# Optimization experiments

Measured on AMD Instinct MI355X. Metric: run time of the kernel, lower is better.

The kernel has to match this reference:

```python
import jax, jax.numpy as jnp
import numpy as np
from jax import lax

THRESHOLDS = (0.25, 0.5, 0.75)
TAU = 100.0
NUM_CLASSES = 10
K = 32
RES_Z = 5.0
# each of the 16 binary logic gates is bilinear: g(a,b) = c0 + c1*a + c2*b + c3*a*b
GATE_COEF = jnp.array([
    [0, 0, 0, 0],   # 0: False
    [0, 0, 0, 1],   # 1: a AND b
    [0, 1, 0, -1],  # 2: a AND NOT b
    [0, 1, 0, 0],   # 3: a  (residual gate)
    [0, 0, 1, -1],  # 4: NOT a AND b
    [0, 0, 1, 0],   # 5: b
    [0, 1, 1, -2],  # 6: XOR
    [0, 1, 1, -1],  # 7: OR
    [1, -1, -1, 1], # 8: NOR
    [1, -1, -1, 2], # 9: XNOR
    [1, 0, -1, 0],  # 10: NOT b
    [1, 0, -1, 1],  # 11: a OR NOT b
    [1, -1, 0, 0],  # 12: NOT a
    [1, -1, 0, 1],  # 13: NOT a OR b
    [1, 0, 0, -1],  # 14: NAND
    [1, 0, 0, 0],   # 15: True
], dtype=jnp.float32)


def _gate_logits(key, shape):
    # residual init: pass-through gate (id 3) dominates
    w = 0.01 * jax.random.normal(key, shape, dtype=jnp.float32)
    return w.at[..., 3].add(RES_Z)


def _leaf_idx(rng, C, O, leaves=8, cpt=2, kk=9):
    # each tree uses cpt random input channels; each leaf picks one of them and a 3x3 position
    ch2 = rng.integers(0, C, size=(O, cpt))
    sel = rng.integers(0, cpt, size=(O, leaves))
    ch = np.take_along_axis(ch2, sel, axis=1)
    pos = rng.integers(0, kk, size=(O, leaves))
    return jnp.asarray(ch * kk + pos, dtype=jnp.int32)


def setup_inputs() -> dict:
    key = jax.random.key(0)
    ks = jax.random.split(key, 9)
    rng = np.random.default_rng(0)
    B = 128
    d = {"x": jax.random.uniform(ks[0], (B, 3, 32, 32), dtype=jnp.float32)}
    in_chs = [3 * len(THRESHOLDS), K, 4 * K, 16 * K]
    out_chs = [K, 4 * K, 16 * K, 32 * K]
    for i, (ci, co) in enumerate(zip(in_chs, out_chs)):
        d[f"c{i+1}_idx"] = _leaf_idx(rng, ci, co)
        d[f"c{i+1}_w"] = _gate_logits(ks[1 + i], (co, 7, 16))
    dims = [32 * K * 4, 1280 * K, 640 * K, 320 * K]
    for i in range(3):
        di, do = dims[i], dims[i + 1]
        d[f"l{i+1}_a"] = jnp.asarray(rng.integers(0, di, size=(do,)), dtype=jnp.int32)
        d[f"l{i+1}_b"] = jnp.asarray(rng.integers(0, di, size=(do,)), dtype=jnp.int32)
        d[f"l{i+1}_w"] = _gate_logits(ks[5 + i], (do, 16))
    return d


def _mix(logits):
    # softmax over 16 gates folded into 4 bilinear coefficients (fused gate mixture)
    return jax.nn.softmax(logits, axis=-1) @ GATE_COEF


def binarize(x):
    return jnp.concatenate([(x > t).astype(x.dtype) for t in THRESHOLDS], axis=1)


def tree_conv(x, leaf_idx, logits):
    # x: (B,C,H,W); leaf_idx: (O,8) into C*9 channel-major patch; logits: (O,7,16)
    B, C, H, W = x.shape
    xp = jnp.pad(x, ((0, 0), (0, 0), (1, 1), (1, 1)))
    patches = jnp.stack([xp[:, :, i:i + H, j:j + W] for i in range(3) for j in range(3)], axis=2)
    patches = patches.reshape(B, C * 9, H, W)
    vals = patches[:, leaf_idx]  # (B,O,8,H,W)
    m = _mix(logits)             # (O,7,4)
    node = 0
    for lvl in (4, 2, 1):
        a, b = vals[:, :, 0::2], vals[:, :, 1::2]
        w = m[:, node:node + lvl]  # (O,lvl,4)
        w0 = w[..., 0][None, :, :, None, None]
        w1 = w[..., 1][None, :, :, None, None]
        w2 = w[..., 2][None, :, :, None, None]
        w3 = w[..., 3][None, :, :, None, None]
        vals = w0 + w1 * a + w2 * b + w3 * (a * b)
        node += lvl
    return vals[:, :, 0]  # (B,O,H,W)


def or_pool(x):
    # OR of relaxed binary values == max pool 2x2/2
    return lax.reduce_window(x, -jnp.inf, lax.max, (1, 1, 2, 2), (1, 1, 2, 2), "VALID")


def logic_layer(x, a_idx, b_idx, logits):
    a = x[:, a_idx]  # (B,O)
    b = x[:, b_idx]
    w = _mix(logits)  # (O,4)
    return w[:, 0] + w[:, 1] * a + w[:, 2] * b + w[:, 3] * (a * b)


def group_sum(x):
    B = x.shape[0]
    return x.reshape(B, NUM_CLASSES, -1).sum(axis=-1) / TAU


def reference(x, c1_idx, c1_w, c2_idx, c2_w, c3_idx, c3_w, c4_idx, c4_w,
              l1_a, l1_b, l1_w, l2_a, l2_b, l2_w, l3_a, l3_b, l3_w):
    h = binarize(x)
    h = or_pool(tree_conv(h, c1_idx, c1_w))
    h = or_pool(tree_conv(h, c2_idx, c2_w))
    h = or_pool(tree_conv(h, c3_idx, c3_w))
    h = or_pool(tree_conv(h, c4_idx, c4_w))
    h = h.reshape(h.shape[0], -1)  # (B, 4096)
    h = logic_layer(h, l1_a, l1_b, l1_w)
    h = logic_layer(h, l2_a, l2_b, l2_w)
    h = logic_layer(h, l3_a, l3_b, l3_w)
    return group_sum(h)  # (B, 10)
```

## Files before the change

### kernel.cpp

```cpp
#include <hip/hip_runtime.h>

#define BATCH 128

typedef float v2f __attribute__((ext_vector_type(2)));
typedef float v4f __attribute__((ext_vector_type(4)));

__device__ __constant__ float GC[16][4] = {
  {0,0,0,0},{0,0,0,1},{0,1,0,-1},{0,1,0,0},
  {0,0,1,-1},{0,0,1,0},{0,1,1,-2},{0,1,1,-1},
  {1,-1,-1,1},{1,-1,-1,2},{1,0,-1,0},{1,0,-1,1},
  {1,-1,0,0},{1,-1,0,1},{1,0,0,-1},{1,0,0,0}};

__device__ __forceinline__ v2f pk_mul(v2f a, v2f b) {
  v2f d;
  asm("v_pk_mul_f32 %0, %1, %2" : "=v"(d) : "v"(a), "v"(b));
  return d;
}
__device__ __forceinline__ v2f max2(v2f a, v2f b) {
  v2f d;
  d.x = fmaxf(a.x, b.x);
  d.y = fmaxf(a.y, b.y);
  return d;
}
__device__ __forceinline__ v2f gate2pk(v2f a, v2f b, v2f w01, v2f w23) {
  v2f t = pk_mul(a, b);
  v2f d;
  asm("v_pk_fma_f32 %0, %1, %2, %2 op_sel:[0,1,0] op_sel_hi:[1,1,0]"
      : "=v"(d) : "v"(a), "v"(w01));
  asm("v_pk_fma_f32 %0, %1, %2, %0 op_sel:[0,0,0] op_sel_hi:[1,0,1]"
      : "+v"(d) : "v"(b), "v"(w23));
  asm("v_pk_fma_f32 %0, %1, %2, %0 op_sel:[0,1,0] op_sel_hi:[1,1,1]"
      : "+v"(d) : "v"(t), "v"(w23));
  return d;
}

__device__ __forceinline__ void mix_one(const float* lp, float* op) {
  float e[16];
  float s = 0.f;
  #pragma unroll
  for (int i = 0; i < 16; ++i) { e[i] = __expf(lp[i]); s += e[i]; }
  float inv = 1.0f / s;
  float w0 = 0.f, w1 = 0.f, w2 = 0.f, w3 = 0.f;
  #pragma unroll
  for (int i = 0; i < 16; ++i) {
    float p = e[i] * inv;
    w0 = fmaf(p, GC[i][0], w0);
    w1 = fmaf(p, GC[i][1], w1);
    w2 = fmaf(p, GC[i][2], w2);
    w3 = fmaf(p, GC[i][3], w3);
  }
  op[0] = w0; op[1] = w1; op[2] = w2; op[3] = w3;
}

struct PrepArgs {
  const float* x;
  const float* logits[7];
  float* outm[7];
  float* xtb;
  float* out;
};

__global__ __launch_bounds__(256) void prep_k(PrepArgs A) {
  __shared__ float tile[64 * 129];
  int blk = blockIdx.x;
  if (blk < 327) {
    int gid = blk * 256 + threadIdx.x;
    const int n[7] = {224, 896, 3584, 7168, 40960, 20480, 10240};
    if (gid < 83552) {
      int g = gid, seg = 0;
      while (seg < 6 && g >= n[seg]) { g -= n[seg]; ++seg; }
      mix_one(A.logits[seg] + (size_t)g * 16, A.outm[seg] + (size_t)g * 4);
    }
  } else if (blk < 327 + 144) {
    int tb = blk - 327;
    int c    = tb / 16;
    int pix0 = (tb % 16) * 64;
    int ti = c / 3, rgb = c - ti * 3;
    float th = 0.25f * (float)(ti + 1);
    {
      int pix = threadIdx.x & 63;
      int b0  = threadIdx.x >> 6;
      #pragma unroll 4
      for (int i = 0; i < 32; ++i) {
        int b = b0 + i * 4;
        float xv = A.x[(size_t)(b * 3 + rgb) * 1024 + pix0 + pix];
        tile[pix * 129 + b] = (xv > th) ? 1.f : 0.f;
      }
    }
    __syncthreads();
    {
      int b  = threadIdx.x & 127;
      int p0 = threadIdx.x >> 7;
      #pragma unroll 4
      for (int i = 0; i < 32; ++i) {
        int pix = p0 + i * 2;
        A.xtb[(size_t)(c * 1024 + pix0 + pix) * BATCH + b] = tile[pix * 129 + b];
      }
    }
  } else {
    int t = threadIdx.x;
    #pragma unroll
    for (int i = 0; i < 5; ++i) A.out[t * 5 + i] = 0.f;
  }
}

template <int H, int W>
__global__ __launch_bounds__(256) void conv_t(
    const float* __restrict__ in_t, const int* __restrict__ li_g,
    const float* __restrict__ m, float* __restrict__ out_t) {
  constexpr int PH = H / 2, PWD = W / 2, PIX = PH * PWD;
  int wave = threadIdx.x >> 6;
  int b2   = threadIdx.x & 63;
  int q = __builtin_amdgcn_readfirstlane(blockIdx.x * 4 + wave);
  int o = q / PIX;
  int p = q - o * PIX;
  int ph = p / PWD;
  int pw = p - ph * PWD;

  const int* li = li_g + o * 8;
  const v4f* mv = (const v4f*)(m + o * 28);
  v4f g0 = mv[0], g1 = mv[1], g2 = mv[2], g3 = mv[3];
  v4f g4 = mv[4], g5 = mv[5], g6 = mv[6];

  v2f best = {-1e30f, -1e30f};
  #pragma unroll
  for (int half = 0; half < 2; ++half) {
    v2f v[2][8];
    #pragma unroll
    for (int l = 0; l < 8; ++l) {
      int idx = li[l];
      int c = idx / 9;
      int k = idx - c * 9;
      int di = k / 3 - 1;
      int dj = (k - (k / 3) * 3) - 1;
      const float* base = in_t + (size_t)(c * H * W) * BATCH;
      int y = 2 * ph + half + di;
      #pragma unroll
      for (int pi = 0; pi < 2; ++pi) {
        int x = 2 * pw + pi + dj;
        v2f val = {0.f, 0.f};
        if ((unsigned)y < (unsigned)H && (unsigned)x < (unsigned)W)
          val = ((const v2f*)(base + (size_t)(y * W + x) * BATCH))[b2];
        v[pi][l] = val;
      }
    }
    #pragma unroll
    for (int pi = 0; pi < 2; ++pi) {
      v2f u0 = gate2pk(v[pi][0], v[pi][1], g0.xy, g0.zw);
      v2f u1 = gate2pk(v[pi][2], v[pi][3], g1.xy, g1.zw);
      v2f u2 = gate2pk(v[pi][4], v[pi][5], g2.xy, g2.zw);
      v2f u3 = gate2pk(v[pi][6], v[pi][7], g3.xy, g3.zw);
      v2f s0 = gate2pk(u0, u1, g4.xy, g4.zw);
      v2f s1 = gate2pk(u2, u3, g5.xy, g5.zw);
      v2f r  = gate2pk(s0, s1, g6.xy, g6.zw);
      best = max2(best, r);
    }
  }
  ((v2f*)(out_t + (size_t)q * BATCH))[b2] = best;
}

__global__ __launch_bounds__(256) void logic_k(
    const float* __restrict__ in, const int* __restrict__ aidx,
    const int* __restrict__ bidx, const float* __restrict__ m,
    float* __restrict__ out) {
  int wave = threadIdx.x >> 6;
  int b2   = threadIdx.x & 63;
  int j0 = blockIdx.x * 16 + wave;
  #pragma unroll
  for (int it = 0; it < 4; ++it) {
    int j = __builtin_amdgcn_readfirstlane(j0 + it * 4);
    int ai = aidx[j];
    int bi = bidx[j];
    v4f w = ((const v4f*)m)[j];
    v2f a = ((const v2f*)(in + (size_t)ai * BATCH))[b2];
    v2f b = ((const v2f*)(in + (size_t)bi * BATCH))[b2];
    ((v2f*)(out + (size_t)j * BATCH))[b2] = gate2pk(a, b, w.xy, w.zw);
  }
}

__global__ __launch_bounds__(256) void logic3_gsum_k(
    const float* __restrict__ in, const int* __restrict__ aidx,
    const int* __restrict__ bidx, const float* __restrict__ m,
    float* __restrict__ out) {
  __shared__ v2f red[4][64];
  int wave = threadIdx.x >> 6;
  int b2   = threadIdx.x & 63;
  int base = __builtin_amdgcn_readfirstlane(blockIdx.x * 256 + wave * 64);
  int cls  = base >> 10;
  v2f s = {0.f, 0.f};
  #pragma unroll 4
  for (int it = 0; it < 64; ++it) {
    int j = base + it;
    int ai = aidx[j];
    int bi = bidx[j];
    v4f w = ((const v4f*)m)[j];
    v2f a = ((const v2f*)(in + (size_t)ai * BATCH))[b2];
    v2f b = ((const v2f*)(in + (size_t)bi * BATCH))[b2];
    s += gate2pk(a, b, w.xy, w.zw);
  }
  red[wave][b2] = s;
  __syncthreads();
  if (threadIdx.x < 64) {
    v2f t = red[0][b2] + red[1][b2] + red[2][b2] + red[3][b2];
    atomicAdd(&out[(2 * b2) * 10 + cls], t.x * 0.01f);
    atomicAdd(&out[(2 * b2 + 1) * 10 + cls], t.y * 0.01f);
  }
}

extern "C" void kernel_launch(void* const* d_in, const int* in_sizes, int n_in,
                              void* d_out, int out_size, void* d_ws, size_t ws_size,
                              hipStream_t stream) {
  const float* x   = (const float*)d_in[0];
  const int*   c1i = (const int*)d_in[1];
  const float* c1w = (const float*)d_in[2];
  const int*   c2i = (const int*)d_in[3];
  const float* c2w = (const float*)d_in[4];
  const int*   c3i = (const int*)d_in[5];
  const float* c3w = (const float*)d_in[6];
  const int*   c4i = (const int*)d_in[7];
  const float* c4w = (const float*)d_in[8];
  const int*   l1a = (const int*)d_in[9];
  const int*   l1b = (const int*)d_in[10];
  const float* l1w = (const float*)d_in[11];
  const int*   l2a = (const int*)d_in[12];
  const int*   l2b = (const int*)d_in[13];
  const float* l2w = (const float*)d_in[14];
  const int*   l3a = (const int*)d_in[15];
  const int*   l3b = (const int*)d_in[16];
  const float* l3w = (const float*)d_in[17];

  float* ws = (float*)d_ws;
  float* mc1 = ws;
  float* mc2 = mc1 + 896;
  float* mc3 = mc2 + 3584;
  float* mc4 = mc3 + 14336;
  float* ml1 = mc4 + 28672;
  float* ml2 = ml1 + 163840;
  float* ml3 = ml2 + 81920;
  float* xtb = ml3 + 40960;
  float* h1  = xtb + 1179648;
  float* h2  = h1 + 1048576;
  float* h3  = h2 + 1048576;
  float* h4  = h3 + 1048576;
  float* g1  = h4 + 524288;
  float* g2  = g1 + 5242880;

  PrepArgs A;
  A.x = x;
  A.logits[0] = c1w; A.outm[0] = mc1;
  A.logits[1] = c2w; A.outm[1] = mc2;
  A.logits[2] = c3w; A.outm[2] = mc3;
  A.logits[3] = c4w; A.outm[3] = mc4;
  A.logits[4] = l1w; A.outm[4] = ml1;
  A.logits[5] = l2w; A.outm[5] = ml2;
  A.logits[6] = l3w; A.outm[6] = ml3;
  A.xtb = xtb;
  A.out = (float*)d_out;
  prep_k<<<472, 256, 0, stream>>>(A);

  conv_t<32, 32><<<8192 / 4, 256, 0, stream>>>(xtb, c1i, mc1, h1);
  conv_t<16, 16><<<8192 / 4, 256, 0, stream>>>(h1, c2i, mc2, h2);
  conv_t<8, 8><<<8192 / 4, 256, 0, stream>>>(h2, c3i, mc3, h3);
  conv_t<4, 4><<<4096 / 4, 256, 0, stream>>>(h3, c4i, mc4, h4);

  logic_k<<<40960 / 16, 256, 0, stream>>>(h4, l1a, l1b, ml1, g1);
  logic_k<<<20480 / 16, 256, 0, stream>>>(g1, l2a, l2b, ml2, g2);
  logic3_gsum_k<<<40, 256, 0, stream>>>(g2, l3a, l3b, ml3, (float*)d_out);
}
```

Baseline: 158.2 us.

## Store intermediate activations in fp16 and spread final logic layer over more blocks

All intermediate activation buffers (binarized input, conv outputs, logic layer outputs) are stored as half2 instead of float, which halves the bytes moved by the gather-heavy conv and logic kernels. The conv kernel also remaps block indices in an 8-way interleave to change which output channels and pixels neighbouring blocks handle, likely for cache or channel locality. The final logic+group-sum kernel launches 320 blocks of 8 gates per wave instead of 40 blocks of 64, giving more parallelism at the cost of more atomics. Intermediate values lose precision, since the relaxed gate outputs are rounded to fp16 after every layer.

```diff
diff --git a/kernel.cpp b/kernel.cpp
--- a/kernel.cpp
+++ b/kernel.cpp
@@ -1,4 +1,5 @@
 #include <hip/hip_runtime.h>
+#include <hip/hip_fp16.h>
 
 #define BATCH 128
 
@@ -34,6 +35,15 @@
   return d;
 }
 
+__device__ __forceinline__ v2f h2f(__half2 h) {
+  float2 f = __half22float2(h);
+  return v2f{f.x, f.y};
+}
+__device__ __forceinline__ __half2 f2h(v2f v) {
+  float2 f; f.x = v.x; f.y = v.y;
+  return __float22half2_rn(f);
+}
+
 __device__ __forceinline__ void mix_one(const float* lp, float* op) {
   float e[16];
   float s = 0.f;
@@ -56,7 +66,7 @@
   const float* x;
   const float* logits[7];
   float* outm[7];
-  float* xtb;
+  __half* xtb;
   float* out;
 };
 
@@ -89,12 +99,16 @@
     }
     __syncthreads();
     {
-      int b  = threadIdx.x & 127;
-      int p0 = threadIdx.x >> 7;
+      int b2i = threadIdx.x & 63;
+      int p0  = threadIdx.x >> 6;
       #pragma unroll 4
-      for (int i = 0; i < 32; ++i) {
-        int pix = p0 + i * 2;
-        A.xtb[(size_t)(c * 1024 + pix0 + pix) * BATCH + b] = tile[pix * 129 + b];
+      for (int i = 0; i < 16; ++i) {
+        int pix = p0 + i * 4;
+        float lo = tile[pix * 129 + 2 * b2i];
+        float hi = tile[pix * 129 + 2 * b2i + 1];
+        float2 f; f.x = lo; f.y = hi;
+        ((__half2*)A.xtb)[(size_t)(c * 1024 + pix0 + pix) * 64 + b2i] =
+            __float22half2_rn(f);
       }
     }
   } else {
@@ -106,12 +120,14 @@
 
 template <int H, int W>
 __global__ __launch_bounds__(256) void conv_t(
-    const float* __restrict__ in_t, const int* __restrict__ li_g,
-    const float* __restrict__ m, float* __restrict__ out_t) {
+    const __half* __restrict__ in_t, const int* __restrict__ li_g,
+    const float* __restrict__ m, __half* __restrict__ out_t) {
   constexpr int PH = H / 2, PWD = W / 2, PIX = PH * PWD;
   int wave = threadIdx.x >> 6;
   int b2   = threadIdx.x & 63;
-  int q = __builtin_amdgcn_readfirstlane(blockIdx.x * 4 + wave);
+  int nb8  = gridDim.x >> 3;
+  int sb   = (blockIdx.x & 7) * nb8 + (blockIdx.x >> 3);
+  int q = __builtin_amdgcn_readfirstlane(sb * 4 + wave);
   int o = q / PIX;
   int p = q - o * PIX;
   int ph = p / PWD;
@@ -121,6 +137,8 @@
   const v4f* mv = (const v4f*)(m + o * 28);
   v4f g0 = mv[0], g1 = mv[1], g2 = mv[2], g3 = mv[3];
   v4f g4 = mv[4], g5 = mv[5], g6 = mv[6];
+
+  const __half2* in2 = (const __half2*)in_t;
 
   v2f best = {-1e30f, -1e30f};
   #pragma unroll
@@ -133,14 +151,13 @@
       int k = idx - c * 9;
       int di = k / 3 - 1;
       int dj = (k - (k / 3) * 3) - 1;
-      const float* base = in_t + (size_t)(c * H * W) * BATCH;
       int y = 2 * ph + half + di;
       #pragma unroll
       for (int pi = 0; pi < 2; ++pi) {
         int x = 2 * pw + pi + dj;
         v2f val = {0.f, 0.f};
         if ((unsigned)y < (unsigned)H && (unsigned)x < (unsigned)W)
-          val = ((const v2f*)(base + (size_t)(y * W + x) * BATCH))[b2];
+          val = h2f(in2[(size_t)(c * H * W + y * W + x) * 64 + b2]);
         v[pi][l] = val;
       }
     }
@@ -156,46 +173,48 @@
       best = max2(best, r);
     }
   }
-  ((v2f*)(out_t + (size_t)q * BATCH))[b2] = best;
+  ((__half2*)out_t)[(size_t)q * 64 + b2] = f2h(best);
 }
 
 __global__ __launch_bounds__(256) void logic_k(
-    const float* __restrict__ in, const int* __restrict__ aidx,
+    const __half* __restrict__ in, const int* __restrict__ aidx,
     const int* __restrict__ bidx, const float* __restrict__ m,
-    float* __restrict__ out) {
+    __half* __restrict__ out) {
   int wave = threadIdx.x >> 6;
   int b2   = threadIdx.x & 63;
   int j0 = blockIdx.x * 16 + wave;
+  const __half2* in2 = (const __half2*)in;
   #pragma unroll
   for (int it = 0; it < 4; ++it) {
     int j = __builtin_amdgcn_readfirstlane(j0 + it * 4);
     int ai = aidx[j];
     int bi = bidx[j];
     v4f w = ((const v4f*)m)[j];
-    v2f a = ((const v2f*)(in + (size_t)ai * BATCH))[b2];
-    v2f b = ((const v2f*)(in + (size_t)bi * BATCH))[b2];
-    ((v2f*)(out + (size_t)j * BATCH))[b2] = gate2pk(a, b, w.xy, w.zw);
+    v2f a = h2f(in2[(size_t)ai * 64 + b2]);
+    v2f b = h2f(in2[(size_t)bi * 64 + b2]);
+    ((__half2*)out)[(size_t)j * 64 + b2] = f2h(gate2pk(a, b, w.xy, w.zw));
   }
 }
 
 __global__ __launch_bounds__(256) void logic3_gsum_k(
-    const float* __restrict__ in, const int* __restrict__ aidx,
+    const __half* __restrict__ in, const int* __restrict__ aidx,
     const int* __restrict__ bidx, const float* __restrict__ m,
     float* __restrict__ out) {
   __shared__ v2f red[4][64];
   int wave = threadIdx.x >> 6;
   int b2   = threadIdx.x & 63;
-  int base = __builtin_amdgcn_readfirstlane(blockIdx.x * 256 + wave * 64);
+  int base = __builtin_amdgcn_readfirstlane(blockIdx.x * 32 + wave * 8);
   int cls  = base >> 10;
+  const __half2* in2 = (const __half2*)in;
   v2f s = {0.f, 0.f};
-  #pragma unroll 4
-  for (int it = 0; it < 64; ++it) {
+  #pragma unroll
+  for (int it = 0; it < 8; ++it) {
     int j = base + it;
     int ai = aidx[j];
     int bi = bidx[j];
     v4f w = ((const v4f*)m)[j];
-    v2f a = ((const v2f*)(in + (size_t)ai * BATCH))[b2];
-    v2f b = ((const v2f*)(in + (size_t)bi * BATCH))[b2];
+    v2f a = h2f(in2[(size_t)ai * 64 + b2]);
+    v2f b = h2f(in2[(size_t)bi * 64 + b2]);
     s += gate2pk(a, b, w.xy, w.zw);
   }
   red[wave][b2] = s;
@@ -237,13 +256,13 @@
   float* ml1 = mc4 + 28672;
   float* ml2 = ml1 + 163840;
   float* ml3 = ml2 + 81920;
-  float* xtb = ml3 + 40960;
-  float* h1  = xtb + 1179648;
-  float* h2  = h1 + 1048576;
-  float* h3  = h2 + 1048576;
-  float* h4  = h3 + 1048576;
-  float* g1  = h4 + 524288;
-  float* g2  = g1 + 5242880;
+  __half* xtb = (__half*)(ml3 + 40960);
+  __half* h1  = xtb + 1179648;
+  __half* h2  = h1 + 1048576;
+  __half* h3  = h2 + 1048576;
+  __half* h4  = h3 + 1048576;
+  __half* g1  = h4 + 524288;
+  __half* g2  = g1 + 5242880;
 
   PrepArgs A;
   A.x = x;
@@ -265,5 +284,5 @@
 
   logic_k<<<40960 / 16, 256, 0, stream>>>(h4, l1a, l1b, ml1, g1);
   logic_k<<<20480 / 16, 256, 0, stream>>>(g1, l2a, l2b, ml2, g2);
-  logic3_gsum_k<<<40, 256, 0, stream>>>(g2, l3a, l3b, ml3, (float*)d_out);
-}
+  logic3_gsum_k<<<320, 256, 0, stream>>>(g2, l3a, l3b, ml3, (float*)d_out);
+}
```

Result: slower. 183.5 us (+16.0%).

## Process four batch elements per lane and two outputs per wave in all kernels

Applied to the files above, without the earlier changes.

Each lane now loads and computes a float4 of batch values instead of float2, so one wave covers two pooled output pixels (conv) or two gate outputs (logic), halving grid sizes. Conv blocks are also remapped with an 8-way interleave of block indices, presumably for locality across channels. The final logic/group-sum kernel is split across more blocks, with a smaller per-wave loop and a revised reduction. Wider loads cut instruction count per byte, but each lane holds more live registers and fewer waves are available to hide latency.

```diff
diff --git a/kernel.cpp b/kernel.cpp
--- a/kernel.cpp
+++ b/kernel.cpp
@@ -14,12 +14,6 @@
 __device__ __forceinline__ v2f pk_mul(v2f a, v2f b) {
   v2f d;
   asm("v_pk_mul_f32 %0, %1, %2" : "=v"(d) : "v"(a), "v"(b));
-  return d;
-}
-__device__ __forceinline__ v2f max2(v2f a, v2f b) {
-  v2f d;
-  d.x = fmaxf(a.x, b.x);
-  d.y = fmaxf(a.y, b.y);
   return d;
 }
 __device__ __forceinline__ v2f gate2pk(v2f a, v2f b, v2f w01, v2f w23) {
@@ -31,6 +25,20 @@
       : "+v"(d) : "v"(b), "v"(w23));
   asm("v_pk_fma_f32 %0, %1, %2, %0 op_sel:[0,1,0] op_sel_hi:[1,1,1]"
       : "+v"(d) : "v"(t), "v"(w23));
+  return d;
+}
+__device__ __forceinline__ v4f gate4pk(v4f a, v4f b, v2f w01, v2f w23) {
+  v4f r;
+  r.xy = gate2pk(a.xy, b.xy, w01, w23);
+  r.zw = gate2pk(a.zw, b.zw, w01, w23);
+  return r;
+}
+__device__ __forceinline__ v4f max4(v4f a, v4f b) {
+  v4f d;
+  d.x = fmaxf(a.x, b.x);
+  d.y = fmaxf(a.y, b.y);
+  d.z = fmaxf(a.z, b.z);
+  d.w = fmaxf(a.w, b.w);
   return d;
 }
 
@@ -110,22 +118,32 @@
     const float* __restrict__ m, float* __restrict__ out_t) {
   constexpr int PH = H / 2, PWD = W / 2, PIX = PH * PWD;
   int wave = threadIdx.x >> 6;
-  int b2   = threadIdx.x & 63;
-  int q = __builtin_amdgcn_readfirstlane(blockIdx.x * 4 + wave);
-  int o = q / PIX;
-  int p = q - o * PIX;
-  int ph = p / PWD;
-  int pw = p - ph * PWD;
+  int lane = threadIdx.x & 63;
+  int half_id = lane >> 5;
+  int b4      = lane & 31;
+  int nb8  = gridDim.x >> 3;
+  int sb   = (blockIdx.x & 7) * nb8 + (blockIdx.x >> 3);
+  int t = __builtin_amdgcn_readfirstlane(sb * 4 + wave);
+  int q0 = 2 * t;
+  int o  = q0 / PIX;
+  int p0 = q0 - o * PIX;
+  int ph = p0 / PWD;
+  int pw0 = p0 - ph * PWD;
 
   const int* li = li_g + o * 8;
   const v4f* mv = (const v4f*)(m + o * 28);
   v4f g0 = mv[0], g1 = mv[1], g2 = mv[2], g3 = mv[3];
   v4f g4 = mv[4], g5 = mv[5], g6 = mv[6];
 
-  v2f best = {-1e30f, -1e30f};
+  int px    = 2 * half_id;
+  int vlane = half_id * 64 + b4;
+
+  const v4f* in4 = (const v4f*)in_t;
+
+  v4f best = {-1e30f, -1e30f, -1e30f, -1e30f};
   #pragma unroll
   for (int half = 0; half < 2; ++half) {
-    v2f v[2][8];
+    v4f v[2][8];
     #pragma unroll
     for (int l = 0; l < 8; ++l) {
       int idx = li[l];
@@ -133,30 +151,31 @@
       int k = idx - c * 9;
       int di = k / 3 - 1;
       int dj = (k - (k / 3) * 3) - 1;
-      const float* base = in_t + (size_t)(c * H * W) * BATCH;
       int y = 2 * ph + half + di;
+      int rowb = c * (H * W) + y * W;
       #pragma unroll
       for (int pi = 0; pi < 2; ++pi) {
-        int x = 2 * pw + pi + dj;
-        v2f val = {0.f, 0.f};
+        int sx = 2 * pw0 + pi + dj;
+        int x  = sx + px;
+        v4f val = {0.f, 0.f, 0.f, 0.f};
         if ((unsigned)y < (unsigned)H && (unsigned)x < (unsigned)W)
-          val = ((const v2f*)(base + (size_t)(y * W + x) * BATCH))[b2];
+          val = in4[(ptrdiff_t)(rowb + sx) * 32 + vlane];
         v[pi][l] = val;
       }
     }
     #pragma unroll
     for (int pi = 0; pi < 2; ++pi) {
-      v2f u0 = gate2pk(v[pi][0], v[pi][1], g0.xy, g0.zw);
-      v2f u1 = gate2pk(v[pi][2], v[pi][3], g1.xy, g1.zw);
-      v2f u2 = gate2pk(v[pi][4], v[pi][5], g2.xy, g2.zw);
-      v2f u3 = gate2pk(v[pi][6], v[pi][7], g3.xy, g3.zw);
-      v2f s0 = gate2pk(u0, u1, g4.xy, g4.zw);
-      v2f s1 = gate2pk(u2, u3, g5.xy, g5.zw);
-      v2f r  = gate2pk(s0, s1, g6.xy, g6.zw);
-      best = max2(best, r);
-    }
-  }
-  ((v2f*)(out_t + (size_t)q * BATCH))[b2] = best;
+      v4f u0 = gate4pk(v[pi][0], v[pi][1], g0.xy, g0.zw);
+      v4f u1 = gate4pk(v[pi][2], v[pi][3], g1.xy, g1.zw);
+      v4f u2 = gate4pk(v[pi][4], v[pi][5], g2.xy, g2.zw);
+      v4f u3 = gate4pk(v[pi][6], v[pi][7], g3.xy, g3.zw);
+      v4f s0 = gate4pk(u0, u1, g4.xy, g4.zw);
+      v4f s1 = gate4pk(u2, u3, g5.xy, g5.zw);
+      v4f r  = gate4pk(s0, s1, g6.xy, g6.zw);
+      best = max4(best, r);
+    }
+  }
+  ((v4f*)out_t)[(size_t)q0 * 32 + half_id * 32 + b4] = best;
 }
 
 __global__ __launch_bounds__(256) void logic_k(
@@ -164,17 +183,20 @@
     const int* __restrict__ bidx, const float* __restrict__ m,
     float* __restrict__ out) {
   int wave = threadIdx.x >> 6;
-  int b2   = threadIdx.x & 63;
-  int j0 = blockIdx.x * 16 + wave;
+  int lane = threadIdx.x & 63;
+  int half_id = lane >> 5;
+  int b4      = lane & 31;
+  int jb = blockIdx.x * 32 + wave * 2;
+  const v4f* in4 = (const v4f*)in;
   #pragma unroll
   for (int it = 0; it < 4; ++it) {
-    int j = __builtin_amdgcn_readfirstlane(j0 + it * 4);
-    int ai = aidx[j];
-    int bi = bidx[j];
-    v4f w = ((const v4f*)m)[j];
-    v2f a = ((const v2f*)(in + (size_t)ai * BATCH))[b2];
-    v2f b = ((const v2f*)(in + (size_t)bi * BATCH))[b2];
-    ((v2f*)(out + (size_t)j * BATCH))[b2] = gate2pk(a, b, w.xy, w.zw);
+    int jj = jb + it * 8 + half_id;
+    int ai = aidx[jj];
+    int bi = bidx[jj];
+    v4f w = ((const v4f*)m)[jj];
+    v4f a = in4[(size_t)ai * 32 + b4];
+    v4f b = in4[(size_t)bi * 32 + b4];
+    ((v4f*)out)[(size_t)jj * 32 + b4] = gate4pk(a, b, w.xy, w.zw);
   }
 }
 
@@ -182,28 +204,34 @@
     const float* __restrict__ in, const int* __restrict__ aidx,
     const int* __restrict__ bidx, const float* __restrict__ m,
     float* __restrict__ out) {
-  __shared__ v2f red[4][64];
+  __shared__ v4f red[4][64];
   int wave = threadIdx.x >> 6;
-  int b2   = threadIdx.x & 63;
-  int base = __builtin_amdgcn_readfirstlane(blockIdx.x * 256 + wave * 64);
+  int lane = threadIdx.x & 63;
+  int half_id = lane >> 5;
+  int b4      = lane & 31;
+  int base = __builtin_amdgcn_readfirstlane(blockIdx.x * 32 + wave * 8);
   int cls  = base >> 10;
-  v2f s = {0.f, 0.f};
-  #pragma unroll 4
-  for (int it = 0; it < 64; ++it) {
-    int j = base + it;
+  const v4f* in4 = (const v4f*)in;
+  v4f s = {0.f, 0.f, 0.f, 0.f};
+  #pragma unroll
+  for (int it = 0; it < 4; ++it) {
+    int j = base + half_id * 4 + it;
     int ai = aidx[j];
     int bi = bidx[j];
     v4f w = ((const v4f*)m)[j];
-    v2f a = ((const v2f*)(in + (size_t)ai * BATCH))[b2];
-    v2f b = ((const v2f*)(in + (size_t)bi * BATCH))[b2];
-    s += gate2pk(a, b, w.xy, w.zw);
-  }
-  red[wave][b2] = s;
+    v4f a = in4[(size_t)ai * 32 + b4];
+    v4f b = in4[(size_t)bi * 32 + b4];
+    s += gate4pk(a, b, w.xy, w.zw);
+  }
+  red[wave][lane] = s;
   __syncthreads();
-  if (threadIdx.x < 64) {
-    v2f t = red[0][b2] + red[1][b2] + red[2][b2] + red[3][b2];
-    atomicAdd(&out[(2 * b2) * 10 + cls], t.x * 0.01f);
-    atomicAdd(&out[(2 * b2 + 1) * 10 + cls], t.y * 0.01f);
+  if (threadIdx.x < 32) {
+    v4f t = {0.f, 0.f, 0.f, 0.f};
+    #pragma unroll
+    for (int w = 0; w < 4; ++w) t += red[w][threadIdx.x] + red[w][threadIdx.x + 32];
+    #pragma unroll
+    for (int i = 0; i < 4; ++i)
+      atomicAdd(&out[(4 * threadIdx.x + i) * 10 + cls], t[i] * 0.01f);
   }
 }
 
@@ -258,12 +286,12 @@
   A.out = (float*)d_out;
   prep_k<<<472, 256, 0, stream>>>(A);
 
-  conv_t<32, 32><<<8192 / 4, 256, 0, stream>>>(xtb, c1i, mc1, h1);
-  conv_t<16, 16><<<8192 / 4, 256, 0, stream>>>(h1, c2i, mc2, h2);
-  conv_t<8, 8><<<8192 / 4, 256, 0, stream>>>(h2, c3i, mc3, h3);
-  conv_t<4, 4><<<4096 / 4, 256, 0, stream>>>(h3, c4i, mc4, h4);
-
-  logic_k<<<40960 / 16, 256, 0, stream>>>(h4, l1a, l1b, ml1, g1);
-  logic_k<<<20480 / 16, 256, 0, stream>>>(g1, l2a, l2b, ml2, g2);
-  logic3_gsum_k<<<40, 256, 0, stream>>>(g2, l3a, l3b, ml3, (float*)d_out);
-}
+  conv_t<32, 32><<<8192 / 8, 256, 0, stream>>>(xtb, c1i, mc1, h1);
+  conv_t<16, 16><<<8192 / 8, 256, 0, stream>>>(h1, c2i, mc2, h2);
+  conv_t<8, 8><<<8192 / 8, 256, 0, stream>>>(h2, c3i, mc3, h3);
+  conv_t<4, 4><<<4096 / 8, 256, 0, stream>>>(h3, c4i, mc4, h4);
+
+  logic_k<<<40960 / 32, 256, 0, stream>>>(h4, l1a, l1b, ml1, g1);
+  logic_k<<<20480 / 32, 256, 0, stream>>>(g1, l2a, l2b, ml2, g2);
+  logic3_gsum_k<<<320, 256, 0, stream>>>(g2, l3a, l3b, ml3, (float*)d_out);
+}
```

Result: no change. 157.3 us (-0.6%).

## Fuse all conv and logic layers into one per-sample LDS-resident megakernel

Applied to the files above, without the earlier changes.

Replaces the chain of eight global-memory kernels with a single kernel in which one 512-thread block processes one batch sample. All activations stay in shared memory, using halo-padded buffers so bounds checks disappear and precomputed leaf offsets. Logic-layer activations are kept in fp16 to fit in LDS, and the group sum is reduced in-block with no global atomics. This removes inter-kernel launches and global round trips, but exposes only 128 blocks of parallelism and adds fp16 rounding to intermediate values.

```diff
diff --git a/kernel.cpp b/kernel.cpp
--- a/kernel.cpp
+++ b/kernel.cpp
@@ -1,9 +1,9 @@
 #include <hip/hip_runtime.h>
-
-#define BATCH 128
+#include <hip/hip_fp16.h>
 
 typedef float v2f __attribute__((ext_vector_type(2)));
 typedef float v4f __attribute__((ext_vector_type(4)));
+typedef int   v4i __attribute__((ext_vector_type(4)));
 
 __device__ __constant__ float GC[16][4] = {
   {0,0,0,0},{0,0,0,1},{0,1,0,-1},{0,1,0,0},
@@ -14,12 +14,6 @@
 __device__ __forceinline__ v2f pk_mul(v2f a, v2f b) {
   v2f d;
   asm("v_pk_mul_f32 %0, %1, %2" : "=v"(d) : "v"(a), "v"(b));
-  return d;
-}
-__device__ __forceinline__ v2f max2(v2f a, v2f b) {
-  v2f d;
-  d.x = fmaxf(a.x, b.x);
-  d.y = fmaxf(a.y, b.y);
   return d;
 }
 __device__ __forceinline__ v2f gate2pk(v2f a, v2f b, v2f w01, v2f w23) {
@@ -53,158 +47,208 @@
 }
 
 struct PrepArgs {
-  const float* x;
   const float* logits[7];
   float* outm[7];
-  float* xtb;
+  const int* cidx[4];
+  int* offt[4];
+};
+
+__global__ __launch_bounds__(256) void prep_k(PrepArgs A) {
+  int gid = blockIdx.x * 256 + threadIdx.x;
+  if (gid < 83552) {
+    const int n[7] = {224, 896, 3584, 7168, 40960, 20480, 10240};
+    int g = gid, seg = 0;
+    while (seg < 6 && g >= n[seg]) { g -= n[seg]; ++seg; }
+    mix_one(A.logits[seg] + (size_t)g * 16, A.outm[seg] + (size_t)g * 4);
+  } else if (gid < 85248) {
+    int r = gid - 83552;
+    int L, rr, H;
+    if (r < 32)       { L = 0; rr = r;       H = 32; }
+    else if (r < 160) { L = 1; rr = r - 32;  H = 16; }
+    else if (r < 672) { L = 2; rr = r - 160; H = 8;  }
+    else              { L = 3; rr = r - 672; H = 4;  }
+    const int* ci = A.cidx[L] + rr * 8;
+    int* oo = A.offt[L] + rr * 8;
+    int W2 = H + 2;
+    #pragma unroll
+    for (int l = 0; l < 8; ++l) {
+      int idx = ci[l];
+      int c  = idx / 9;
+      int k  = idx - 9 * c;
+      int di = k / 3 - 1;
+      int dj = k - 3 * (k / 3) - 1;
+      oo[l] = (c * (H + 2) + 1 + di) * W2 + 1 + dj;
+    }
+  }
+}
+
+struct MegaArgs {
+  const float* x;
+  const float* mc[4];
+  const int*   offt[4];
+  const int*   la[3];
+  const int*   lb[3];
+  const float* mlw[3];
   float* out;
 };
 
-__global__ __launch_bounds__(256) void prep_k(PrepArgs A) {
-  __shared__ float tile[64 * 129];
-  int blk = blockIdx.x;
-  if (blk < 327) {
-    int gid = blk * 256 + threadIdx.x;
-    const int n[7] = {224, 896, 3584, 7168, 40960, 20480, 10240};
-    if (gid < 83552) {
-      int g = gid, seg = 0;
-      while (seg < 6 && g >= n[seg]) { g -= n[seg]; ++seg; }
-      mix_one(A.logits[seg] + (size_t)g * 16, A.outm[seg] + (size_t)g * 4);
-    }
-  } else if (blk < 327 + 144) {
-    int tb = blk - 327;
-    int c    = tb / 16;
-    int pix0 = (tb % 16) * 64;
-    int ti = c / 3, rgb = c - ti * 3;
-    float th = 0.25f * (float)(ti + 1);
-    {
-      int pix = threadIdx.x & 63;
-      int b0  = threadIdx.x >> 6;
-      #pragma unroll 4
-      for (int i = 0; i < 32; ++i) {
-        int b = b0 + i * 4;
-        float xv = A.x[(size_t)(b * 3 + rgb) * 1024 + pix0 + pix];
-        tile[pix * 129 + b] = (xv > th) ? 1.f : 0.f;
-      }
-    }
-    __syncthreads();
-    {
-      int b  = threadIdx.x & 127;
-      int p0 = threadIdx.x >> 7;
-      #pragma unroll 4
-      for (int i = 0; i < 32; ++i) {
-        int pix = p0 + i * 2;
-        A.xtb[(size_t)(c * 1024 + pix0 + pix) * BATCH + b] = tile[pix * 129 + b];
-      }
-    }
-  } else {
-    int t = threadIdx.x;
-    #pragma unroll
-    for (int i = 0; i < 5; ++i) A.out[t * 5 + i] = 0.f;
-  }
-}
-
-template <int H, int W>
-__global__ __launch_bounds__(256) void conv_t(
-    const float* __restrict__ in_t, const int* __restrict__ li_g,
-    const float* __restrict__ m, float* __restrict__ out_t) {
-  constexpr int PH = H / 2, PWD = W / 2, PIX = PH * PWD;
-  int wave = threadIdx.x >> 6;
-  int b2   = threadIdx.x & 63;
-  int q = __builtin_amdgcn_readfirstlane(blockIdx.x * 4 + wave);
-  int o = q / PIX;
-  int p = q - o * PIX;
-  int ph = p / PWD;
-  int pw = p - ph * PWD;
-
-  const int* li = li_g + o * 8;
-  const v4f* mv = (const v4f*)(m + o * 28);
-  v4f g0 = mv[0], g1 = mv[1], g2 = mv[2], g3 = mv[3];
-  v4f g4 = mv[4], g5 = mv[5], g6 = mv[6];
-
-  v2f best = {-1e30f, -1e30f};
-  #pragma unroll
-  for (int half = 0; half < 2; ++half) {
-    v2f v[2][8];
+extern __shared__ char S[];
+
+template<int OH, int OW, int LOGOW, int IW2, int PIXCNT, int LOGPIX,
+         int NCH, int ITERS, bool UNI, bool HALO>
+__device__ __forceinline__ void conv_stage(
+    const float* in, float* outb,
+    const int* __restrict__ offt, const float* __restrict__ mtab, int tid) {
+  int pix = tid & (PIXCNT - 1);
+  int ch0 = tid >> LOGPIX;
+  int pw  = pix & (OW - 1);
+  int ph  = pix >> LOGOW;
+  int pixbase = (2 * ph) * IW2 + 2 * pw;
+  #pragma unroll 2
+  for (int it = 0; it < ITERS; ++it) {
+    int ch = ch0 + NCH * it;
+    if (UNI) ch = __builtin_amdgcn_readfirstlane(ch);
+    const int* ot = offt + ch * 8;
+    const float* mt = mtab + ch * 28;
+    v4f g0 = *(const v4f*)(mt +  0);
+    v4f g1 = *(const v4f*)(mt +  4);
+    v4f g2 = *(const v4f*)(mt +  8);
+    v4f g3 = *(const v4f*)(mt + 12);
+    v4f g4 = *(const v4f*)(mt + 16);
+    v4f g5 = *(const v4f*)(mt + 20);
+    v4f g6 = *(const v4f*)(mt + 24);
+    v2f v01[8], v23[8];
     #pragma unroll
     for (int l = 0; l < 8; ++l) {
-      int idx = li[l];
-      int c = idx / 9;
-      int k = idx - c * 9;
-      int di = k / 3 - 1;
-      int dj = (k - (k / 3) * 3) - 1;
-      const float* base = in_t + (size_t)(c * H * W) * BATCH;
-      int y = 2 * ph + half + di;
+      int a0 = ot[l] + pixbase;
+      v2f t0; t0.x = in[a0];       t0.y = in[a0 + 1];
+      v2f t1; t1.x = in[a0 + IW2]; t1.y = in[a0 + IW2 + 1];
+      v01[l] = t0; v23[l] = t1;
+    }
+    v2f u0 = gate2pk(v01[0], v01[1], g0.xy, g0.zw);
+    v2f u1 = gate2pk(v01[2], v01[3], g1.xy, g1.zw);
+    v2f u2 = gate2pk(v01[4], v01[5], g2.xy, g2.zw);
+    v2f u3 = gate2pk(v01[6], v01[7], g3.xy, g3.zw);
+    v2f s0 = gate2pk(u0, u1, g4.xy, g4.zw);
+    v2f s1 = gate2pk(u2, u3, g5.xy, g5.zw);
+    v2f r0 = gate2pk(s0, s1, g6.xy, g6.zw);
+    u0 = gate2pk(v23[0], v23[1], g0.xy, g0.zw);
+    u1 = gate2pk(v23[2], v23[3], g1.xy, g1.zw);
+    u2 = gate2pk(v23[4], v23[5], g2.xy, g2.zw);
+    u3 = gate2pk(v23[6], v23[7], g3.xy, g3.zw);
+    s0 = gate2pk(u0, u1, g4.xy, g4.zw);
+    s1 = gate2pk(u2, u3, g5.xy, g5.zw);
+    v2f r1 = gate2pk(s0, s1, g6.xy, g6.zw);
+    float res = fmaxf(fmaxf(r0.x, r0.y), fmaxf(r1.x, r1.y));
+    if (HALO)
+      outb[ch * (OH + 2) * (OW + 2) + (1 + ph) * (OW + 2) + 1 + pw] = res;
+    else
+      outb[ch * (OH * OW) + pix] = res;
+  }
+}
+
+__global__ __launch_bounds__(512, 2) void mega_k(MegaArgs A) {
+  int tid = threadIdx.x;
+  int b = blockIdx.x;
+  float* binb = (float*)(S);
+  float* buf1 = (float*)(S + 53248);
+  float* buf2 = (float*)(S);
+  float* buf3 = (float*)(S + 53248);
+  float* h4   = (float*)(S);
+  __half* g1h = (__half*)(S + 16384);
+  __half* g2h = (__half*)(S + 98304);
+  float* lsum = (float*)(S + 139264);
+
+  for (int i = tid; i < 10404; i += 512) binb[i] = 0.f;
+  if (tid < 10) lsum[tid] = 0.f;
+  __syncthreads();
+  const float* xb = A.x + (size_t)b * 3072;
+  #pragma unroll
+  for (int i = 0; i < 6; ++i) {
+    int idx = tid + 512 * i;
+    float v = xb[idx];
+    int rgb = idx >> 10;
+    int rem = idx & 1023;
+    int y = rem >> 5, xx = rem & 31;
+    int base = (1 + y) * 34 + 1 + xx;
+    binb[(0 + rgb) * 1156 + base] = v > 0.25f ? 1.f : 0.f;
+    binb[(3 + rgb) * 1156 + base] = v > 0.50f ? 1.f : 0.f;
+    binb[(6 + rgb) * 1156 + base] = v > 0.75f ? 1.f : 0.f;
+  }
+  __syncthreads();
+
+  for (int i = tid; i < 10368; i += 512) buf1[i] = 0.f;
+  __syncthreads();
+  conv_stage<16,16,4,34,256,8,2,16,true,true>(binb, buf1, A.offt[0], A.mc[0], tid);
+  __syncthreads();
+  for (int i = tid; i < 12800; i += 512) buf2[i] = 0.f;
+  __syncthreads();
+  conv_stage<8,8,3,18,64,6,8,16,true,true>(buf1, buf2, A.offt[1], A.mc[1], tid);
+  __syncthreads();
+  for (int i = tid; i < 18432; i += 512) buf3[i] = 0.f;
+  __syncthreads();
+  conv_stage<4,4,2,10,16,4,32,16,false,true>(buf2, buf3, A.offt[2], A.mc[2], tid);
+  __syncthreads();
+  conv_stage<2,2,1,6,4,2,128,8,false,false>(buf3, h4, A.offt[3], A.mc[3], tid);
+  __syncthreads();
+
+  {
+    const v4i* a4 = (const v4i*)A.la[0];
+    const v4i* b4 = (const v4i*)A.lb[0];
+    const v4f* w4 = (const v4f*)A.mlw[0];
+    #pragma unroll 2
+    for (int g = 0; g < 20; ++g) {
+      int q = tid + 512 * g;
+      v4i ai = a4[q], bi = b4[q];
       #pragma unroll
-      for (int pi = 0; pi < 2; ++pi) {
-        int x = 2 * pw + pi + dj;
-        v2f val = {0.f, 0.f};
-        if ((unsigned)y < (unsigned)H && (unsigned)x < (unsigned)W)
-          val = ((const v2f*)(base + (size_t)(y * W + x) * BATCH))[b2];
-        v[pi][l] = val;
+      for (int i = 0; i < 4; ++i) {
+        v4f w = w4[4 * q + i];
+        float a = h4[ai[i]], bb = h4[bi[i]];
+        g1h[4 * q + i] = __float2half(fmaf(w.w, a * bb, fmaf(w.z, bb, fmaf(w.y, a, w.x))));
       }
     }
+  }
+  __syncthreads();
+  {
+    const v4i* a4 = (const v4i*)A.la[1];
+    const v4i* b4 = (const v4i*)A.lb[1];
+    const v4f* w4 = (const v4f*)A.mlw[1];
+    #pragma unroll 2
+    for (int g = 0; g < 10; ++g) {
+      int q = tid + 512 * g;
+      v4i ai = a4[q], bi = b4[q];
+      #pragma unroll
+      for (int i = 0; i < 4; ++i) {
+        v4f w = w4[4 * q + i];
+        float a = __half2float(g1h[ai[i]]), bb = __half2float(g2h == 0 ? g1h[bi[i]] : g1h[bi[i]]);
+        g2h[4 * q + i] = __float2half(fmaf(w.w, a * bb, fmaf(w.z, bb, fmaf(w.y, a, w.x))));
+      }
+    }
+  }
+  __syncthreads();
+  {
+    const v4i* a4 = (const v4i*)A.la[2];
+    const v4i* b4 = (const v4i*)A.lb[2];
+    const v4f* w4 = (const v4f*)A.mlw[2];
+    int wv = tid >> 6, lane = tid & 63;
     #pragma unroll
-    for (int pi = 0; pi < 2; ++pi) {
-      v2f u0 = gate2pk(v[pi][0], v[pi][1], g0.xy, g0.zw);
-      v2f u1 = gate2pk(v[pi][2], v[pi][3], g1.xy, g1.zw);
-      v2f u2 = gate2pk(v[pi][4], v[pi][5], g2.xy, g2.zw);
-      v2f u3 = gate2pk(v[pi][6], v[pi][7], g3.xy, g3.zw);
-      v2f s0 = gate2pk(u0, u1, g4.xy, g4.zw);
-      v2f s1 = gate2pk(u2, u3, g5.xy, g5.zw);
-      v2f r  = gate2pk(s0, s1, g6.xy, g6.zw);
-      best = max2(best, r);
-    }
-  }
-  ((v2f*)(out_t + (size_t)q * BATCH))[b2] = best;
-}
-
-__global__ __launch_bounds__(256) void logic_k(
-    const float* __restrict__ in, const int* __restrict__ aidx,
-    const int* __restrict__ bidx, const float* __restrict__ m,
-    float* __restrict__ out) {
-  int wave = threadIdx.x >> 6;
-  int b2   = threadIdx.x & 63;
-  int j0 = blockIdx.x * 16 + wave;
-  #pragma unroll
-  for (int it = 0; it < 4; ++it) {
-    int j = __builtin_amdgcn_readfirstlane(j0 + it * 4);
-    int ai = aidx[j];
-    int bi = bidx[j];
-    v4f w = ((const v4f*)m)[j];
-    v2f a = ((const v2f*)(in + (size_t)ai * BATCH))[b2];
-    v2f b = ((const v2f*)(in + (size_t)bi * BATCH))[b2];
-    ((v2f*)(out + (size_t)j * BATCH))[b2] = gate2pk(a, b, w.xy, w.zw);
-  }
-}
-
-__global__ __launch_bounds__(256) void logic3_gsum_k(
-    const float* __restrict__ in, const int* __restrict__ aidx,
-    const int* __restrict__ bidx, const float* __restrict__ m,
-    float* __restrict__ out) {
-  __shared__ v2f red[4][64];
-  int wave = threadIdx.x >> 6;
-  int b2   = threadIdx.x & 63;
-  int base = __builtin_amdgcn_readfirstlane(blockIdx.x * 256 + wave * 64);
-  int cls  = base >> 10;
-  v2f s = {0.f, 0.f};
-  #pragma unroll 4
-  for (int it = 0; it < 64; ++it) {
-    int j = base + it;
-    int ai = aidx[j];
-    int bi = bidx[j];
-    v4f w = ((const v4f*)m)[j];
-    v2f a = ((const v2f*)(in + (size_t)ai * BATCH))[b2];
-    v2f b = ((const v2f*)(in + (size_t)bi * BATCH))[b2];
-    s += gate2pk(a, b, w.xy, w.zw);
-  }
-  red[wave][b2] = s;
-  __syncthreads();
-  if (threadIdx.x < 64) {
-    v2f t = red[0][b2] + red[1][b2] + red[2][b2] + red[3][b2];
-    atomicAdd(&out[(2 * b2) * 10 + cls], t.x * 0.01f);
-    atomicAdd(&out[(2 * b2 + 1) * 10 + cls], t.y * 0.01f);
-  }
+    for (int g = 0; g < 5; ++g) {
+      int q = tid + 512 * g;
+      v4i ai = a4[q], bi = b4[q];
+      float s = 0.f;
+      #pragma unroll
+      for (int i = 0; i < 4; ++i) {
+        v4f w = w4[4 * q + i];
+        float a = __half2float(g2h[ai[i]]), bb = __half2float(g2h[bi[i]]);
+        s += fmaf(w.w, a * bb, fmaf(w.z, bb, fmaf(w.y, a, w.x)));
+      }
+      #pragma unroll
+      for (int m = 1; m < 64; m <<= 1) s += __shfl_xor(s, m);
+      if (lane == 0) atomicAdd(&lsum[(wv + 8 * g) >> 2], s);
+    }
+  }
+  __syncthreads();
+  if (tid < 10) A.out[b * 10 + tid] = lsum[tid] * 0.01f;
 }
 
 extern "C" void kernel_launch(void* const* d_in, const int* in_sizes, int n_in,
@@ -237,33 +281,39 @@
   float* ml1 = mc4 + 28672;
   float* ml2 = ml1 + 163840;
   float* ml3 = ml2 + 81920;
-  float* xtb = ml3 + 40960;
-  float* h1  = xtb + 1179648;
-  float* h2  = h1 + 1048576;
-  float* h3  = h2 + 1048576;
-  float* h4  = h3 + 1048576;
-  float* g1  = h4 + 524288;
-  float* g2  = g1 + 5242880;
-
-  PrepArgs A;
-  A.x = x;
-  A.logits[0] = c1w; A.outm[0] = mc1;
-  A.logits[1] = c2w; A.outm[1] = mc2;
-  A.logits[2] = c3w; A.outm[2] = mc3;
-  A.logits[3] = c4w; A.outm[3] = mc4;
-  A.logits[4] = l1w; A.outm[4] = ml1;
-  A.logits[5] = l2w; A.outm[5] = ml2;
-  A.logits[6] = l3w; A.outm[6] = ml3;
-  A.xtb = xtb;
-  A.out = (float*)d_out;
-  prep_k<<<472, 256, 0, stream>>>(A);
-
-  conv_t<32, 32><<<8192 / 4, 256, 0, stream>>>(xtb, c1i, mc1, h1);
-  conv_t<16, 16><<<8192 / 4, 256, 0, stream>>>(h1, c2i, mc2, h2);
-  conv_t<8, 8><<<8192 / 4, 256, 0, stream>>>(h2, c3i, mc3, h3);
-  conv_t<4, 4><<<4096 / 4, 256, 0, stream>>>(h3, c4i, mc4, h4);
-
-  logic_k<<<40960 / 16, 256, 0, stream>>>(h4, l1a, l1b, ml1, g1);
-  logic_k<<<20480 / 16, 256, 0, stream>>>(g1, l2a, l2b, ml2, g2);
-  logic3_gsum_k<<<40, 256, 0, stream>>>(g2, l3a, l3b, ml3, (float*)d_out);
-}
+  int* off1 = (int*)(ml3 + 40960);
+  int* off2 = off1 + 256;
+  int* off3 = off2 + 1024;
+  int* off4 = off3 + 4096;
+
+  PrepArgs P;
+  P.logits[0] = c1w; P.outm[0] = mc1;
+  P.logits[1] = c2w; P.outm[1] = mc2;
+  P.logits[2] = c3w; P.outm[2] = mc3;
+  P.logits[3] = c4w; P.outm[3] = mc4;
+  P.logits[4] = l1w; P.outm[4] = ml1;
+  P.logits[5] = l2w; P.outm[5] = ml2;
+  P.logits[6] = l3w; P.outm[6] = ml3;
+  P.cidx[0] = c1i; P.offt[0] = off1;
+  P.cidx[1] = c2i; P.offt[1] = off2;
+  P.cidx[2] = c3i; P.offt[2] = off3;
+  P.cidx[3] = c4i; P.offt[3] = off4;
+  prep_k<<<333, 256, 0, stream>>>(P);
+
+  MegaArgs M;
+  M.x = x;
+  M.mc[0] = mc1; M.mc[1] = mc2; M.mc[2] = mc3; M.mc[3] = mc4;
+  M.offt[0] = off1; M.offt[1] = off2; M.offt[2] = off3; M.offt[3] = off4;
+  M.la[0] = l1a; M.lb[0] = l1b; M.mlw[0] = ml1;
+  M.la[1] = l2a; M.lb[1] = l2b; M.mlw[1] = ml2;
+  M.la[2] = l3a; M.lb[2] = l3b; M.mlw[2] = ml3;
+  M.out = (float*)d_out;
+
+  static bool attr_set = false;
+  if (!attr_set) {
+    hipFuncSetAttribute((const void*)mega_k,
+                        hipFuncAttributeMaxDynamicSharedMemorySize, 139328);
+    attr_set = true;
+  }
+  mega_k<<<128, 512, 139328, stream>>>(M);
+}
```

After: 161.1 us. No clear change (+1.8%).
